# Optimization experiments

Hardware: AMD Instinct MI355X
Metric: run time of the kernel (lower is better)

## Reference

```python
import jax, jax.numpy as jnp
import numpy as np
import math

B, S, H, D = 4, 2048, 16, 64
HID = H * D  # 1024


def setup_inputs() -> dict:
    key = jax.random.key(0)
    ks = jax.random.split(key, 9)
    s_in = 1.0 / math.sqrt(D)
    s_hid = 1.0 / math.sqrt(HID)
    return {
        "x": jax.random.normal(ks[0], (B, S, D), dtype=jnp.float32),
        "Wq": jax.random.uniform(ks[1], (D, HID), jnp.float32, -s_in, s_in),
        "bq": jax.random.uniform(ks[2], (HID,), jnp.float32, -s_in, s_in),
        "Wk": jax.random.uniform(ks[3], (D, HID), jnp.float32, -s_in, s_in),
        "bk": jax.random.uniform(ks[4], (HID,), jnp.float32, -s_in, s_in),
        "Wv": jax.random.uniform(ks[5], (D, HID), jnp.float32, -s_in, s_in),
        "bv": jax.random.uniform(ks[6], (HID,), jnp.float32, -s_in, s_in),
        "Wo": jax.random.uniform(ks[7], (HID, D), jnp.float32, -s_hid, s_hid),
        "bo": jax.random.uniform(ks[8], (D,), jnp.float32, -s_hid, s_hid),
    }


def reference(x, Wq, bq, Wk, bk, Wv, bv, Wo, bo):
    b, s, _ = x.shape
    # projections: [B,S,D] -> [B,S,HID] -> [B,H,S,D]
    q = (x @ Wq + bq).reshape(b, s, H, D).transpose(0, 2, 1, 3)
    k = (x @ Wk + bk).reshape(b, s, H, D).transpose(0, 2, 1, 3)
    v = (x @ Wv + bv).reshape(b, s, H, D).transpose(0, 2, 1, 3)
    scores = jnp.einsum("bhqd,bhkd->bhqk", q, k) / math.sqrt(D)
    # causal mask: -inf strictly above the diagonal
    causal = jnp.tril(jnp.ones((s, s), dtype=bool))
    scores = jnp.where(causal, scores, -jnp.inf)
    attn = jax.nn.softmax(scores, axis=-1)  # dropout is identity at eval
    out = jnp.einsum("bhqk,bhkd->bhqd", attn, v)
    out = out.transpose(0, 2, 1, 3).reshape(b, s, HID)
    return out @ Wo + bo  # [B,S,D]
```

## Files before the change

kernel.cpp:

```cpp
#include <hip/hip_runtime.h>
#include <hip/hip_bf16.h>

#define B 4
#define S 2048
#define H 16
#define D 64
#define HID 1024

typedef __hip_bfloat16 bf16;
typedef __attribute__((ext_vector_type(8))) short bf16x8;
typedef __attribute__((ext_vector_type(4))) short bf16x4;
typedef __attribute__((ext_vector_type(4))) float f32x4;

static __device__ __forceinline__ float b2f(bf16 v) { return __bfloat162float(v); }

static __device__ __forceinline__ unsigned pkbf(float a, float b) {
    union { bf16 h; unsigned short u; } ua, ub;
    ua.h = __float2bfloat16(a);
    ub.h = __float2bfloat16(b);
    return (unsigned)ua.u | ((unsigned)ub.u << 16);
}

#define SCL 0.18033688011112042f

#define QSTR 72

__global__ __launch_bounds__(256) void qkv_mfma_kernel(
    const float* __restrict__ x,
    const float* __restrict__ Wq, const float* __restrict__ bq,
    const float* __restrict__ Wk, const float* __restrict__ bk,
    const float* __restrict__ Wv, const float* __restrict__ bv,
    bf16* __restrict__ q, bf16* __restrict__ k, bf16* __restrict__ v)
{
    __shared__ bf16 Xs[128 * QSTR];
    __shared__ bf16 Wt[128 * QSTR];
    __shared__ float bs[128];

    const int tid = threadIdx.x;
    const int mat = blockIdx.y >> 3;
    const int N0  = (blockIdx.y & 7) * 128;
    const int m0  = blockIdx.x * 128;

    const float* W    = (mat == 0) ? Wq : (mat == 1) ? Wk : Wv;
    const float* bias = (mat == 0) ? bq : (mat == 1) ? bk : bv;
    bf16*        dst  = (mat == 0) ? q  : (mat == 1) ? k  : v;
    const float  oscale = (mat == 0) ? SCL : 1.0f;

    #pragma unroll
    for (int i = 0; i < 8; ++i) {
        int item = i * 256 + tid;
        int row = item >> 4, f4 = item & 15;
        float4 xv = *(const float4*)&x[(size_t)(m0 + row) * D + f4 * 4];
        union { bf16 h[4]; bf16x4 v4; } u;
        u.h[0] = __float2bfloat16(xv.x); u.h[1] = __float2bfloat16(xv.y);
        u.h[2] = __float2bfloat16(xv.z); u.h[3] = __float2bfloat16(xv.w);
        *(bf16x4*)&Xs[row * QSTR + f4 * 4] = u.v4;
    }
    #pragma unroll
    for (int i = 0; i < 2; ++i) {
        int unit = i * 256 + tid;
        int n0 = (unit & 31) * 4, k0 = (unit >> 5) * 4;
        float wv[4][4];
        #pragma unroll
        for (int j = 0; j < 4; ++j) {
            float4 t = *(const float4*)&W[(size_t)(k0 + j) * HID + N0 + n0];
            wv[j][0] = t.x; wv[j][1] = t.y; wv[j][2] = t.z; wv[j][3] = t.w;
        }
        #pragma unroll
        for (int dn = 0; dn < 4; ++dn) {
            union { bf16 h[4]; bf16x4 v4; } u;
            #pragma unroll
            for (int j = 0; j < 4; ++j) u.h[j] = __float2bfloat16(wv[j][dn]);
            *(bf16x4*)&Wt[(n0 + dn) * QSTR + k0] = u.v4;
        }
    }
    if (tid < 128) bs[tid] = bias[N0 + tid];
    __syncthreads();

    const int lane = tid & 63, wave = tid >> 6;
    const int c = lane & 15, quad = lane >> 4;

    bf16x8 af[2][2];
    #pragma unroll
    for (int mg = 0; mg < 2; ++mg)
        #pragma unroll
        for (int kc = 0; kc < 2; ++kc)
            af[mg][kc] = *(const bf16x8*)&Xs[(wave * 32 + mg * 16 + c) * QSTR + kc * 32 + quad * 8];

    f32x4 acc[2][8];
    #pragma unroll
    for (int mg = 0; mg < 2; ++mg)
        #pragma unroll
        for (int ng = 0; ng < 8; ++ng)
            acc[mg][ng] = (f32x4){0.f, 0.f, 0.f, 0.f};

    #pragma unroll
    for (int ng = 0; ng < 8; ++ng) {
        bf16x8 bf0 = *(const bf16x8*)&Wt[(ng * 16 + c) * QSTR + quad * 8];
        bf16x8 bf1 = *(const bf16x8*)&Wt[(ng * 16 + c) * QSTR + 32 + quad * 8];
        #pragma unroll
        for (int mg = 0; mg < 2; ++mg) {
            acc[mg][ng] = __builtin_amdgcn_mfma_f32_16x16x32_bf16(af[mg][0], bf0, acc[mg][ng], 0, 0, 0);
            acc[mg][ng] = __builtin_amdgcn_mfma_f32_16x16x32_bf16(af[mg][1], bf1, acc[mg][ng], 0, 0, 0);
        }
    }

    if (mat == 2) {
        #pragma unroll
        for (int ng = 0; ng < 8; ++ng) {
            int n_g = N0 + ng * 16 + c;
            int h = n_g >> 6, dd = n_g & 63;
            float bb_ = bs[ng * 16 + c];
            #pragma unroll
            for (int mg = 0; mg < 2; ++mg) {
                int row0 = m0 + wave * 32 + mg * 16 + quad * 4;
                int b_ = row0 >> 11, ss = row0 & (S - 1);
                union { bf16 h4[4]; bf16x4 v4; } u;
                #pragma unroll
                for (int r = 0; r < 4; ++r)
                    u.h4[r] = __float2bfloat16(acc[mg][ng][r] + bb_);
                *(bf16x4*)&dst[((size_t)(b_ * H + h) * D + dd) * S + ss] = u.v4;
            }
        }
    } else {
        #pragma unroll
        for (int ng = 0; ng < 8; ++ng) {
            int n_g = N0 + ng * 16 + c;
            int h = n_g >> 6, dd = n_g & 63;
            float bb_ = bs[ng * 16 + c];
            #pragma unroll
            for (int mg = 0; mg < 2; ++mg) {
                #pragma unroll
                for (int r = 0; r < 4; ++r) {
                    int row = m0 + wave * 32 + mg * 16 + quad * 4 + r;
                    int b_ = row >> 11, ss = row & (S - 1);
                    dst[((size_t)(b_ * H + h) * S + ss) * D + dd] =
                        __float2bfloat16((acc[mg][ng][r] + bb_) * oscale);
                }
            }
        }
    }
}

#define BT   64
#define NT   (S / BT)
#define KSTR 72
#define PST  72

__global__ __launch_bounds__(256) void flash_mfma_kernel(
    const bf16* __restrict__ qg, const bf16* __restrict__ kg,
    const bf16* __restrict__ vg, bf16* __restrict__ og)
{
    __shared__ bf16 Ks[BT * KSTR];
    __shared__ bf16 Vt[BT * KSTR];
    __shared__ bf16 Ps[4][16 * PST];

    const int tid  = threadIdx.x;
    const int wave = tid >> 6;
    const int lane = tid & 63;
    const int c    = lane & 15;
    const int quad = lane >> 4;

    const int L    = (int)blockIdx.x + 16 * (int)blockIdx.y;
    const int xcd  = L & 7;
    const int slot = L >> 3;
    const int pair = slot & 15;
    const int bh   = xcd * 8 + (slot >> 4);
    const int b_   = bh >> 4, h_ = bh & 15;
    const size_t hbase = (size_t)bh * S * D;
    bf16* myPs = &Ps[wave][0];
    const int srow = wave * 16 + c;

    const int qta = pair;
    const int qtb = NT - 1 - pair;

    const int sr0 = tid >> 3,         sc0 = (tid & 7) * 8;
    const int sr1 = (tid + 256) >> 3, sc1 = sc0;

    bf16x8 qfa0, qfa1, qfb0, qfb1;
    {
        const size_t ra = hbase + (size_t)(qta * BT + srow) * D;
        const size_t rb = hbase + (size_t)(qtb * BT + srow) * D;
        qfa0 = *(const bf16x8*)(qg + ra + quad * 8);
        qfa1 = *(const bf16x8*)(qg + ra + 32 + quad * 8);
        qfb0 = *(const bf16x8*)(qg + rb + quad * 8);
        qfb1 = *(const bf16x8*)(qg + rb + 32 + quad * 8);
    }

    bf16x8 kreg0, kreg1, vreg0, vreg1;
    kreg0 = *(const bf16x8*)(kg + hbase + (size_t)sr0 * D + sc0);
    kreg1 = *(const bf16x8*)(kg + hbase + (size_t)sr1 * D + sc1);
    vreg0 = *(const bf16x8*)(vg + hbase + (size_t)sr0 * S + sc0);
    vreg1 = *(const bf16x8*)(vg + hbase + (size_t)sr1 * S + sc1);

    float la = 0.f, lb = 0.f;
    f32x4 ota[4], otb[4];
    #pragma unroll
    for (int jn = 0; jn < 4; ++jn) {
        ota[jn] = (f32x4){0.f, 0.f, 0.f, 0.f};
        otb[jn] = (f32x4){0.f, 0.f, 0.f, 0.f};
    }

    auto tile_step = [&](bf16x8 qf0, bf16x8 qf1, f32x4* ot,
                         float& l1, bool diag) {
        f32x4 st[4];
        #pragma unroll
        for (int jn = 0; jn < 4; ++jn) {
            bf16x8 kf0 = *(const bf16x8*)&Ks[(jn * 16 + c) * KSTR + quad * 8];
            bf16x8 kf1 = *(const bf16x8*)&Ks[(jn * 16 + c) * KSTR + 32 + quad * 8];
            f32x4 s = {0.f, 0.f, 0.f, 0.f};
            s = __builtin_amdgcn_mfma_f32_16x16x32_bf16(kf0, qf0, s, 0, 0, 0);
            s = __builtin_amdgcn_mfma_f32_16x16x32_bf16(kf1, qf1, s, 0, 0, 0);
            st[jn] = s;
        }
        uint2 pk[4];
        #pragma unroll
        for (int jn = 0; jn < 4; ++jn) {
            float p0 = __builtin_amdgcn_exp2f(st[jn][0]);
            float p1 = __builtin_amdgcn_exp2f(st[jn][1]);
            float p2 = __builtin_amdgcn_exp2f(st[jn][2]);
            float p3 = __builtin_amdgcn_exp2f(st[jn][3]);
            if (diag) {
                int col = jn * 16 + quad * 4;
                if (col     > srow) p0 = 0.f;
                if (col + 1 > srow) p1 = 0.f;
                if (col + 2 > srow) p2 = 0.f;
                if (col + 3 > srow) p3 = 0.f;
            }
            l1 += (p0 + p1) + (p2 + p3);
            pk[jn].x = pkbf(p0, p1);
            pk[jn].y = pkbf(p2, p3);
        }
        asm volatile("s_waitcnt lgkmcnt(0)" ::: "memory");
        #pragma unroll
        for (int jn = 0; jn < 4; ++jn)
            *(uint2*)&myPs[c * PST + jn * 16 + quad * 4] = pk[jn];
        asm volatile("s_waitcnt lgkmcnt(0)" ::: "memory");
        #pragma unroll
        for (int kc = 0; kc < 2; ++kc) {
            bf16x8 pf = *(const bf16x8*)&myPs[c * PST + kc * 32 + quad * 8];
            #pragma unroll
            for (int jn = 0; jn < 4; ++jn) {
                bf16x8 vf = *(const bf16x8*)&Vt[(jn * 16 + c) * KSTR + kc * 32 + quad * 8];
                ot[jn] = __builtin_amdgcn_mfma_f32_16x16x32_bf16(vf, pf, ot[jn], 0, 0, 0);
            }
        }
    };

    for (int kt = 0; kt <= qtb; ++kt) {
        __syncthreads();
        *(bf16x8*)&Ks[sr0 * KSTR + sc0] = kreg0;
        *(bf16x8*)&Ks[sr1 * KSTR + sc1] = kreg1;
        *(bf16x8*)&Vt[sr0 * KSTR + sc0] = vreg0;
        *(bf16x8*)&Vt[sr1 * KSTR + sc1] = vreg1;
        __syncthreads();

        if (kt < qtb) {
            const int nb = (kt + 1) * BT;
            kreg0 = *(const bf16x8*)(kg + hbase + (size_t)(nb + sr0) * D + sc0);
            kreg1 = *(const bf16x8*)(kg + hbase + (size_t)(nb + sr1) * D + sc1);
            vreg0 = *(const bf16x8*)(vg + hbase + (size_t)sr0 * S + nb + sc0);
            vreg1 = *(const bf16x8*)(vg + hbase + (size_t)sr1 * S + nb + sc1);
        }

        tile_step(qfb0, qfb1, otb, lb, kt == qtb);
        if (kt <= qta) tile_step(qfa0, qfa1, ota, la, kt == qta);
    }

    {
        float lt = lb;
        lt += __shfl_xor(lt, 16);
        lt += __shfl_xor(lt, 32);
        const float inv = 1.f / lt;
        const size_t obase = ((size_t)(b_ * S + qtb * BT + srow)) * HID + h_ * 64 + quad * 4;
        #pragma unroll
        for (int jn = 0; jn < 4; ++jn) {
            union { bf16 h4[4]; bf16x4 v4; } u;
            #pragma unroll
            for (int r = 0; r < 4; ++r)
                u.h4[r] = __float2bfloat16(otb[jn][r] * inv);
            *(bf16x4*)&og[obase + jn * 16] = u.v4;
        }
    }
    {
        float lt = la;
        lt += __shfl_xor(lt, 16);
        lt += __shfl_xor(lt, 32);
        const float inv = 1.f / lt;
        const size_t obase = ((size_t)(b_ * S + qta * BT + srow)) * HID + h_ * 64 + quad * 4;
        #pragma unroll
        for (int jn = 0; jn < 4; ++jn) {
            union { bf16 h4[4]; bf16x4 v4; } u;
            #pragma unroll
            for (int r = 0; r < 4; ++r)
                u.h4[r] = __float2bfloat16(ota[jn][r] * inv);
            *(bf16x4*)&og[obase + jn * 16] = u.v4;
        }
    }
}

__global__ __launch_bounds__(256) void out_proj_mfma_kernel(
    const bf16* __restrict__ o, const float* __restrict__ Wo,
    const float* __restrict__ bo, float* __restrict__ out)
{
    __shared__ bf16 Os[32 * QSTR];
    __shared__ bf16 Wot[64 * QSTR];
    __shared__ float bos[64];

    const int tid = threadIdx.x;
    const int m0  = blockIdx.x * 32;
    const int lane = tid & 63, wave = tid >> 6;
    const int c = lane & 15, quad = lane >> 4;
    const int mtile = wave >> 1;
    const int ngb   = (wave & 1) * 2;

    if (tid < 64) bos[tid] = bo[tid];

    f32x4 acc[2];
    acc[0] = (f32x4){0.f, 0.f, 0.f, 0.f};
    acc[1] = (f32x4){0.f, 0.f, 0.f, 0.f};

    for (int chunk = 0; chunk < 16; ++chunk) {
        const int k0 = chunk * 64;
        __syncthreads();
        {
            int row = tid >> 3, oct = tid & 7;
            *(bf16x8*)&Os[row * QSTR + oct * 8] =
                *(const bf16x8*)(o + (size_t)(m0 + row) * HID + k0 + oct * 8);
        }
        {
            int n0 = (tid & 15) * 4, kk0 = (tid >> 4) * 4;
            float wv[4][4];
            #pragma unroll
            for (int j = 0; j < 4; ++j) {
                float4 t = *(const float4*)&Wo[(size_t)(k0 + kk0 + j) * 64 + n0];
                wv[j][0] = t.x; wv[j][1] = t.y; wv[j][2] = t.z; wv[j][3] = t.w;
            }
            #pragma unroll
            for (int dn = 0; dn < 4; ++dn) {
                union { bf16 h[4]; bf16x4 v4; } u;
                #pragma unroll
                for (int j = 0; j < 4; ++j) u.h[j] = __float2bfloat16(wv[j][dn]);
                *(bf16x4*)&Wot[(n0 + dn) * QSTR + kk0] = u.v4;
            }
        }
        __syncthreads();

        bf16x8 a0 = *(const bf16x8*)&Os[(mtile * 16 + c) * QSTR + quad * 8];
        bf16x8 a1 = *(const bf16x8*)&Os[(mtile * 16 + c) * QSTR + 32 + quad * 8];
        #pragma unroll
        for (int g = 0; g < 2; ++g) {
            int ng = ngb + g;
            bf16x8 b0 = *(const bf16x8*)&Wot[(ng * 16 + c) * QSTR + quad * 8];
            bf16x8 b1 = *(const bf16x8*)&Wot[(ng * 16 + c) * QSTR + 32 + quad * 8];
            acc[g] = __builtin_amdgcn_mfma_f32_16x16x32_bf16(a0, b0, acc[g], 0, 0, 0);
            acc[g] = __builtin_amdgcn_mfma_f32_16x16x32_bf16(a1, b1, acc[g], 0, 0, 0);
        }
    }

    #pragma unroll
    for (int g = 0; g < 2; ++g) {
        int n = (ngb + g) * 16 + c;
        float bb_ = bos[n];
        #pragma unroll
        for (int r = 0; r < 4; ++r) {
            int row = m0 + mtile * 16 + quad * 4 + r;
            out[(size_t)row * 64 + n] = acc[g][r] + bb_;
        }
    }
}

extern "C" void kernel_launch(void* const* d_in, const int* in_sizes, int n_in,
                              void* d_out, int out_size, void* d_ws, size_t ws_size,
                              hipStream_t stream)
{
    const float* x  = (const float*)d_in[0];
    const float* Wq = (const float*)d_in[1];
    const float* bq = (const float*)d_in[2];
    const float* Wk = (const float*)d_in[3];
    const float* bk = (const float*)d_in[4];
    const float* Wv = (const float*)d_in[5];
    const float* bv = (const float*)d_in[6];
    const float* Wo = (const float*)d_in[7];
    const float* bo = (const float*)d_in[8];

    char* ws = (char*)d_ws;
    const size_t qkv_bytes = (size_t)B * S * HID * sizeof(bf16);
    bf16* qw = (bf16*)(ws);
    bf16* kw = (bf16*)(ws + qkv_bytes);
    bf16* vw = (bf16*)(ws + 2 * qkv_bytes);
    bf16* ow = (bf16*)(ws + 3 * qkv_bytes);

    qkv_mfma_kernel<<<dim3(B * S / 128, 24), 256, 0, stream>>>(
        x, Wq, bq, Wk, bk, Wv, bv, qw, kw, vw);

    flash_mfma_kernel<<<dim3(NT / 2, B * H), 256, 0, stream>>>(qw, kw, vw, ow);

    out_proj_mfma_kernel<<<dim3(B * S / 32), 256, 0, stream>>>(ow, Wo, bo,
                                                               (float*)d_out);
}
```

Baseline: 175.9 us.

## Stage V transpose through LDS and interleave both query tiles' score phases

The QKV projection kernel now writes the transposed V output into a shared-memory tile first, then stores it with coalesced 16-byte writes instead of scattered 8-byte stores. The flash kernel splits each tile step into a score/exp phase and a PV phase, using a separate P buffer per query tile. Both tiles' score phases now run before a single LDS wait, so their MFMA and exp work can overlap, and the extra waitcnt barriers go away. The cost is additional LDS for the second P buffer and extra synchronisation in the V projection path.

```diff
diff --git a/kernel.cpp b/kernel.cpp
--- a/kernel.cpp
+++ b/kernel.cpp
@@ -24,6 +24,7 @@
 #define SCL 0.18033688011112042f
 
 #define QSTR 72
+#define VTS  136
 
 __global__ __launch_bounds__(256) void qkv_mfma_kernel(
     const float* __restrict__ x,
@@ -32,9 +33,10 @@
     const float* __restrict__ Wv, const float* __restrict__ bv,
     bf16* __restrict__ q, bf16* __restrict__ k, bf16* __restrict__ v)
 {
-    __shared__ bf16 Xs[128 * QSTR];
-    __shared__ bf16 Wt[128 * QSTR];
+    __shared__ __align__(16) char smem[36864];
     __shared__ float bs[128];
+    bf16* Xs = (bf16*)smem;
+    bf16* Wt = (bf16*)(smem + 128 * QSTR * 2);
 
     const int tid = threadIdx.x;
     const int mat = blockIdx.y >> 3;
@@ -106,21 +108,31 @@
     }
 
     if (mat == 2) {
+        bf16* T = (bf16*)smem;
+        __syncthreads();
         #pragma unroll
         for (int ng = 0; ng < 8; ++ng) {
-            int n_g = N0 + ng * 16 + c;
-            int h = n_g >> 6, dd = n_g & 63;
-            float bb_ = bs[ng * 16 + c];
+            int hid_l = ng * 16 + c;
+            float bb_ = bs[hid_l];
             #pragma unroll
             for (int mg = 0; mg < 2; ++mg) {
-                int row0 = m0 + wave * 32 + mg * 16 + quad * 4;
-                int b_ = row0 >> 11, ss = row0 & (S - 1);
+                int ss_l = wave * 32 + mg * 16 + quad * 4;
                 union { bf16 h4[4]; bf16x4 v4; } u;
                 #pragma unroll
                 for (int r = 0; r < 4; ++r)
                     u.h4[r] = __float2bfloat16(acc[mg][ng][r] + bb_);
-                *(bf16x4*)&dst[((size_t)(b_ * H + h) * D + dd) * S + ss] = u.v4;
-            }
+                *(bf16x4*)&T[hid_l * VTS + ss_l] = u.v4;
+            }
+        }
+        __syncthreads();
+        const int b_ = m0 >> 11, ss0 = m0 & (S - 1);
+        #pragma unroll
+        for (int pass = 0; pass < 8; ++pass) {
+            int unit = pass * 256 + tid;
+            int dd_l = unit >> 4, u8 = unit & 15;
+            bf16x8 val = *(const bf16x8*)&T[dd_l * VTS + u8 * 8];
+            int h = (N0 >> 6) + (dd_l >> 6), ddg = dd_l & 63;
+            *(bf16x8*)&dst[((size_t)(b_ * H + h) * D + ddg) * S + ss0 + u8 * 8] = val;
         }
     } else {
         #pragma unroll
@@ -153,7 +165,8 @@
 {
     __shared__ bf16 Ks[BT * KSTR];
     __shared__ bf16 Vt[BT * KSTR];
-    __shared__ bf16 Ps[4][16 * PST];
+    __shared__ bf16 PsB[4][16 * PST];
+    __shared__ bf16 PsA[4][16 * PST];
 
     const int tid  = threadIdx.x;
     const int wave = tid >> 6;
@@ -168,7 +181,8 @@
     const int bh   = xcd * 8 + (slot >> 4);
     const int b_   = bh >> 4, h_ = bh & 15;
     const size_t hbase = (size_t)bh * S * D;
-    bf16* myPs = &Ps[wave][0];
+    bf16* myPB = &PsB[wave][0];
+    bf16* myPA = &PsA[wave][0];
     const int srow = wave * 16 + c;
 
     const int qta = pair;
@@ -201,8 +215,7 @@
         otb[jn] = (f32x4){0.f, 0.f, 0.f, 0.f};
     }
 
-    auto tile_step = [&](bf16x8 qf0, bf16x8 qf1, f32x4* ot,
-                         float& l1, bool diag) {
+    auto front = [&](bf16x8 qf0, bf16x8 qf1, bf16* Pdst, float& l1, bool diag) {
         f32x4 st[4];
         #pragma unroll
         for (int jn = 0; jn < 4; ++jn) {
@@ -213,7 +226,6 @@
             s = __builtin_amdgcn_mfma_f32_16x16x32_bf16(kf1, qf1, s, 0, 0, 0);
             st[jn] = s;
         }
-        uint2 pk[4];
         #pragma unroll
         for (int jn = 0; jn < 4; ++jn) {
             float p0 = __builtin_amdgcn_exp2f(st[jn][0]);
@@ -228,17 +240,16 @@
                 if (col + 3 > srow) p3 = 0.f;
             }
             l1 += (p0 + p1) + (p2 + p3);
-            pk[jn].x = pkbf(p0, p1);
-            pk[jn].y = pkbf(p2, p3);
-        }
-        asm volatile("s_waitcnt lgkmcnt(0)" ::: "memory");
-        #pragma unroll
-        for (int jn = 0; jn < 4; ++jn)
-            *(uint2*)&myPs[c * PST + jn * 16 + quad * 4] = pk[jn];
-        asm volatile("s_waitcnt lgkmcnt(0)" ::: "memory");
+            uint2 pk;
+            pk.x = pkbf(p0, p1);
+            pk.y = pkbf(p2, p3);
+            *(uint2*)&Pdst[c * PST + jn * 16 + quad * 4] = pk;
+        }
+    };
+    auto pv = [&](const bf16* Psrc, f32x4* ot) {
         #pragma unroll
         for (int kc = 0; kc < 2; ++kc) {
-            bf16x8 pf = *(const bf16x8*)&myPs[c * PST + kc * 32 + quad * 8];
+            bf16x8 pf = *(const bf16x8*)&Psrc[c * PST + kc * 32 + quad * 8];
             #pragma unroll
             for (int jn = 0; jn < 4; ++jn) {
                 bf16x8 vf = *(const bf16x8*)&Vt[(jn * 16 + c) * KSTR + kc * 32 + quad * 8];
@@ -263,8 +274,12 @@
             vreg1 = *(const bf16x8*)(vg + hbase + (size_t)sr1 * S + nb + sc1);
         }
 
-        tile_step(qfb0, qfb1, otb, lb, kt == qtb);
-        if (kt <= qta) tile_step(qfa0, qfa1, ota, la, kt == qta);
+        const bool withA = (kt <= qta);
+        front(qfb0, qfb1, myPB, lb, kt == qtb);
+        if (withA) front(qfa0, qfa1, myPA, la, kt == qta);
+        asm volatile("s_waitcnt lgkmcnt(0)" ::: "memory");
+        pv(myPB, otb);
+        if (withA) pv(myPA, ota);
     }
 
     {
```

Measured after the change: 172.4 us. About the same (-1.9%).
